# Performance work log

Hardware: AMD Instinct MI355X
Metric: run time of the kernel (lower is better)

The kernel has to match this reference:

```python
import jax, jax.numpy as jnp
import numpy as np

N_NODES = 10000
N_EDGES = 640000
NODE_DIM = 128
TIME_DIM = 64


def setup_inputs() -> dict:
    key = jax.random.key(0)
    ks = jax.random.split(key, 16)
    s = 0.05
    return {
        "h": jax.random.normal(ks[0], (N_NODES, NODE_DIM), jnp.float32),
        "diff_cart": jax.random.normal(ks[1], (N_EDGES, 3), jnp.float32),
        "dist_sq": jax.random.uniform(ks[2], (N_EDGES, 1), jnp.float32),
        "edge_src": jax.random.randint(ks[3], (N_EDGES,), 0, N_NODES),
        "edge_dst": jax.random.randint(ks[4], (N_EDGES,), 0, N_NODES),
        "t_emb_edges": jax.random.normal(ks[5], (N_EDGES, TIME_DIM), jnp.float32),
        "t_emb_nodes": jax.random.normal(ks[6], (N_NODES, TIME_DIM), jnp.float32),
        # edge_mlp: Linear(2*D+1+T -> D), SiLU, Linear(D -> D), SiLU
        "eW1": jax.random.normal(ks[7], (2 * NODE_DIM + 1 + TIME_DIM, NODE_DIM), jnp.float32) * s,
        "eb1": jnp.zeros((NODE_DIM,), jnp.float32),
        "eW2": jax.random.normal(ks[8], (NODE_DIM, NODE_DIM), jnp.float32) * s,
        "eb2": jnp.zeros((NODE_DIM,), jnp.float32),
        # coord_mlp: Linear(D -> D), SiLU, Linear(D -> 1, bias=False)
        "cW1": jax.random.normal(ks[9], (NODE_DIM, NODE_DIM), jnp.float32) * s,
        "cb1": jnp.zeros((NODE_DIM,), jnp.float32),
        "cW2": jax.random.normal(ks[10], (NODE_DIM, 1), jnp.float32) * s,
        # node_mlp: Linear(2*D+T -> D), SiLU, Linear(D -> D)
        "nW1": jax.random.normal(ks[11], (2 * NODE_DIM + TIME_DIM, NODE_DIM), jnp.float32) * s,
        "nb1": jnp.zeros((NODE_DIM,), jnp.float32),
        "nW2": jax.random.normal(ks[12], (NODE_DIM, NODE_DIM), jnp.float32) * s,
        "nb2": jnp.zeros((NODE_DIM,), jnp.float32),
    }


def reference(h, diff_cart, dist_sq, edge_src, edge_dst, t_emb_edges, t_emb_nodes,
              eW1, eb1, eW2, eb2, cW1, cb1, cW2, nW1, nb1, nW2, nb2):
    silu = jax.nn.silu
    n_nodes = h.shape[0]
    # gather + edge MLP: [E, 2D+1+T] -> [E, D]
    edge_in = jnp.concatenate([h[edge_src], h[edge_dst], dist_sq, t_emb_edges], axis=-1)
    m_ij = silu(silu(edge_in @ eW1 + eb1) @ eW2 + eb2)
    # coord MLP -> per-edge scalar weight [E, 1]
    coord_w = silu(m_ij @ cW1 + cb1) @ cW2
    # scatter-add coordinate shift onto source nodes [N, 3]
    coord_update = jax.ops.segment_sum(diff_cart * coord_w, edge_src, num_segments=n_nodes)
    # scatter-add messages onto destination nodes [N, D]
    m_i = jax.ops.segment_sum(m_ij, edge_dst, num_segments=n_nodes)
    # node MLP with residual
    node_in = jnp.concatenate([h, m_i, t_emb_nodes], axis=-1)
    h_update = h + (silu(node_in @ nW1 + nb1) @ nW2 + nb2)
    return h_update, coord_update
```

## Files before the change

kernel.cpp:

```cpp
#include <hip/hip_runtime.h>

typedef __bf16 bf16x8 __attribute__((ext_vector_type(8)));
typedef float f32x4 __attribute__((ext_vector_type(4)));
typedef unsigned short u16;

#define NN 10000
#define NE 640000
#define DIM 128
#define TD 64
#define LDT2 112
#define LDX 136
#define LDH 136

__device__ __forceinline__ u16 f2bf(float f){
    union { float f; unsigned u; } v; v.f = f;
    unsigned r = v.u + 0x7fffu + ((v.u >> 16) & 1u);
    return (u16)(r >> 16);
}
__device__ __forceinline__ unsigned f2bf2(float a, float b){
    unsigned r;
    asm("v_cvt_pk_bf16_f32 %0, %1, %2" : "=v"(r) : "v"(a), "v"(b));
    return r;
}
__device__ __forceinline__ float bfu2f(unsigned hs){
    union { unsigned u; float f; } v; v.u = hs << 16; return v.f;
}
__device__ __forceinline__ float silu_f(float x){ return x / (1.0f + __expf(-x)); }

__device__ __forceinline__ unsigned silu_add3_pk(unsigned xb, unsigned us, unsigned ud){
    float a0 = bfu2f(xb & 0xffffu) + bfu2f(us & 0xffffu) + bfu2f(ud & 0xffffu);
    float a1 = bfu2f(xb >> 16)     + bfu2f(us >> 16)     + bfu2f(ud >> 16);
    return f2bf2(silu_f(a0), silu_f(a1));
}

__global__ __launch_bounds__(256) void k_prep1(
    const float* __restrict__ eW1, const float* __restrict__ nW1,
    const float* __restrict__ eW2, const float* __restrict__ cW1,
    const float* __restrict__ nW2, const int* __restrict__ edst,
    u16* __restrict__ nW1t, u16* __restrict__ eW2t, u16* __restrict__ cW1t,
    u16* __restrict__ nW2t, u16* __restrict__ tWe2,
    u16* __restrict__ eW1tS, u16* __restrict__ eW1tD,
    int* __restrict__ deg, float* __restrict__ m_i, float* __restrict__ coord_out)
{
    int i = blockIdx.x * 256 + threadIdx.x;
    if (i < NE) {
        atomicAdd(&deg[edst[i]], 1);
        *reinterpret_cast<float2*>(m_i + (size_t)i * 2) = make_float2(0.f, 0.f);
    }
    if (i < NN * 3) coord_out[i] = 0.f;

    if (i < 40960) {
        int j = i / 320, k = i - j * 320;
        nW1t[i] = f2bf(nW1[k * DIM + j]);
    } else if (i < 57344) {
        int t = i - 40960; int j = t >> 7, k = t & 127;
        eW2t[t] = f2bf(eW2[k * DIM + j]);
    } else if (i < 73728) {
        int t = i - 57344; int j = t >> 7, k = t & 127;
        cW1t[t] = f2bf(cW1[k * DIM + j]);
    } else if (i < 90112) {
        int t = i - 73728; int j = t >> 7, k = t & 127;
        nW2t[t] = f2bf(nW2[k * DIM + j]);
    } else if (i < 102400) {
        int t = i - 90112; int j = t / 96, k = t - j * 96;
        float v = (k < 64) ? eW1[(257 + k) * DIM + j]
                 : (k == 64) ? eW1[256 * DIM + j] : 0.f;
        tWe2[t] = f2bf(v);
    } else if (i < 118784) {
        int t = i - 102400; int j = t >> 7, k = t & 127;
        eW1tS[t] = f2bf(eW1[k * DIM + j]);
    } else if (i < 135168) {
        int t = i - 118784; int j = t >> 7, k = t & 127;
        eW1tD[t] = f2bf(eW1[(128 + k) * DIM + j]);
    }
}

__global__ __launch_bounds__(256) void k_scan(const int* __restrict__ deg,
                                              int* __restrict__ offs, int* __restrict__ cursor){
    __shared__ int ps[256];
    int t = threadIdx.x;
    int base = t * 40, cnt = 0;
    if (t < 250) for (int i = 0; i < 40; ++i) cnt += deg[base + i];
    ps[t] = cnt; __syncthreads();
    for (int d = 1; d < 256; d <<= 1) {
        int v = (t >= d) ? ps[t - d] : 0;
        __syncthreads();
        ps[t] += v;
        __syncthreads();
    }
    int run = (t > 0) ? ps[t - 1] : 0;
    if (t < 250) for (int i = 0; i < 40; ++i) {
        offs[base + i] = run; cursor[base + i] = run; run += deg[base + i];
    }
    if (t == 0) offs[NN] = NE;
}

__global__ __launch_bounds__(256) void k_prep2(
    const float* __restrict__ h, const float* __restrict__ eb1,
    const u16* __restrict__ eW1tS, const u16* __restrict__ eW1tD,
    const int* __restrict__ esrc, const int* __restrict__ edst,
    const float* __restrict__ dist, const float* __restrict__ diffc,
    int* __restrict__ cursor,
    uint4* __restrict__ epack, float4* __restrict__ diff4,
    u16* __restrict__ H12)
{
    __shared__ u16 Hbuf[64 * LDH];
    const int tid = threadIdx.x;

    if (blockIdx.x < 2500) {
        int i = blockIdx.x * 256 + tid;
        if (i < NE) {
            int d = edst[i];
            int pos = atomicAdd(&cursor[d], 1);
            union { float f; unsigned u; } dv; dv.f = dist[i];
            epack[pos] = make_uint4((unsigned)esrc[i], (unsigned)d, dv.u, (unsigned)i);
            diff4[pos] = make_float4(diffc[(size_t)i * 3 + 0],
                                     diffc[(size_t)i * 3 + 1],
                                     diffc[(size_t)i * 3 + 2], 0.f);
        }
        return;
    }

    const int lane = tid & 63, w = tid >> 6;
    const int lo = lane & 15, hi = lane >> 4;
    const int nbase = (blockIdx.x - 2500) * 64;

    #pragma unroll
    for (int it = 0; it < 8; ++it) {
        int f = it * 256 + tid, e = f >> 5, c = f & 31;
        int node = nbase + e; if (node >= NN) node = NN - 1;
        float4 v = *reinterpret_cast<const float4*>(h + (size_t)node * DIM + c * 4);
        unsigned p0 = f2bf2(v.x, v.y), p1 = f2bf2(v.z, v.w);
        *reinterpret_cast<uint2*>(&Hbuf[e * LDH + c * 4]) = make_uint2(p0, p1);
    }
    __syncthreads();

    const u16* Wt = (w < 2) ? eW1tS : eW1tD;
    const int cc = (w & 1) * 64;
    f32x4 acc[4][4];
    #pragma unroll
    for (int rt = 0; rt < 4; ++rt)
        #pragma unroll
        for (int n = 0; n < 4; ++n) acc[rt][n] = f32x4{0.f,0.f,0.f,0.f};
    for (int ks = 0; ks < 4; ++ks) {
        bf16x8 a[4], b[4];
        #pragma unroll
        for (int rt = 0; rt < 4; ++rt)
            a[rt] = *reinterpret_cast<const bf16x8*>(&Hbuf[(rt*16+lo)*LDH + ks*32 + hi*8]);
        #pragma unroll
        for (int n = 0; n < 4; ++n)
            b[n] = *reinterpret_cast<const bf16x8*>(&Wt[(cc + n*16 + lo)*128 + ks*32 + hi*8]);
        #pragma unroll
        for (int rt = 0; rt < 4; ++rt)
            #pragma unroll
            for (int n = 0; n < 4; ++n)
                acc[rt][n] = __builtin_amdgcn_mfma_f32_16x16x32_bf16(a[rt], b[n], acc[rt][n], 0, 0, 0);
    }
    #pragma unroll
    for (int n = 0; n < 4; ++n) {
        int jloc = cc + n * 16 + lo;
        int j = ((w < 2) ? 0 : 128) + jloc;
        float bias = (w < 2) ? eb1[jloc] : 0.f;
        #pragma unroll
        for (int rt = 0; rt < 4; ++rt)
            #pragma unroll
            for (int r = 0; r < 4; ++r) {
                int node = nbase + rt * 16 + hi * 4 + r;
                if (node < NN) H12[(size_t)node * 256 + j] = f2bf(acc[rt][n][r] + bias);
            }
    }
}

__global__ __launch_bounds__(256, 8) void egnn_edge9(
    const uint4* __restrict__ epack, const float4* __restrict__ diff4,
    const float* __restrict__ tembE,
    const float* __restrict__ eb2, const float* __restrict__ cb1,
    const float* __restrict__ cW2,
    const u16* __restrict__ H12, const u16* __restrict__ tWe2,
    const u16* __restrict__ eW2t, const u16* __restrict__ cW1t,
    float* __restrict__ m_i, float* __restrict__ coord_out)
{
    __shared__ u16 B[64 * LDX];
    __shared__ int seid[64], srcv[64], dstv[64], flags[64];
    __shared__ float cwpart[4][64];

    const int tid = threadIdx.x, lane = tid & 63, w = tid >> 6;
    const int lo = lane & 15, hi = lane >> 4;
    const int bid = (blockIdx.x & 7) * 1250 + (blockIdx.x >> 3);
    const int ebase = bid * 64;
    const int colb = w * 32;
    const int col0 = colb + lo;

    float dl = 0.f;
    if (tid < 64) {
        uint4 ep = epack[ebase + tid];
        srcv[tid] = (int)ep.x;
        dstv[tid] = (int)ep.y;
        union { unsigned u; float f; } dv; dv.u = ep.z;
        dl = dv.f;
        seid[tid] = (int)ep.w;
    }
    __syncthreads();

    if (tid < 64) {
        flags[tid] = (tid == 63) || (dstv[tid] != dstv[tid + 1]);
        uint4 z0 = make_uint4((unsigned)f2bf(dl), 0u, 0u, 0u);
        uint4 zz = make_uint4(0u, 0u, 0u, 0u);
        *reinterpret_cast<uint4*>(&B[tid * LDT2 + 64]) = z0;
        *reinterpret_cast<uint4*>(&B[tid * LDT2 + 72]) = zz;
        *reinterpret_cast<uint4*>(&B[tid * LDT2 + 80]) = zz;
        *reinterpret_cast<uint4*>(&B[tid * LDT2 + 88]) = zz;
    }
    #pragma unroll
    for (int it = 0; it < 4; ++it) {
        int f = it * 256 + tid, e = f >> 4, c = f & 15;
        float4 v = *reinterpret_cast<const float4*>(tembE + (size_t)seid[e] * TD + c * 4);
        unsigned p0 = f2bf2(v.x, v.y), p1 = f2bf2(v.z, v.w);
        *reinterpret_cast<uint2*>(&B[e * LDT2 + c * 4]) = make_uint2(p0, p1);
    }
    __syncthreads();

    f32x4 acc[4][2];
    #pragma unroll
    for (int rt = 0; rt < 4; ++rt)
        #pragma unroll
        for (int n = 0; n < 2; ++n) acc[rt][n] = f32x4{0.f,0.f,0.f,0.f};
    #pragma unroll
    for (int ks = 0; ks < 3; ++ks) {
        bf16x8 a[4], b[2];
        #pragma unroll
        for (int rt = 0; rt < 4; ++rt)
            a[rt] = *reinterpret_cast<const bf16x8*>(&B[(rt*16+lo)*LDT2 + ks*32 + hi*8]);
        #pragma unroll
        for (int n = 0; n < 2; ++n)
            b[n] = *reinterpret_cast<const bf16x8*>(&tWe2[(colb + n*16 + lo)*96 + ks*32 + hi*8]);
        #pragma unroll
        for (int rt = 0; rt < 4; ++rt)
            #pragma unroll
            for (int n = 0; n < 2; ++n)
                acc[rt][n] = __builtin_amdgcn_mfma_f32_16x16x32_bf16(a[rt], b[n], acc[rt][n], 0, 0, 0);
    }
    __syncthreads();

    #pragma unroll
    for (int rt = 0; rt < 4; ++rt)
        #pragma unroll
        for (int n = 0; n < 2; ++n)
            #pragma unroll
            for (int r = 0; r < 4; ++r)
                B[(rt*16 + hi*4 + r) * LDX + colb + n*16 + lo] = f2bf(acc[rt][n][r]);
    __syncthreads();

    {
        int row = tid >> 2, q = tid & 3;
        int sv = srcv[row], dv = dstv[row];
        const uint4* hs = reinterpret_cast<const uint4*>(H12 + (size_t)sv * 256 + q * 32);
        const uint4* hd = reinterpret_cast<const uint4*>(H12 + (size_t)dv * 256 + 128 + q * 32);
        uint4* bp = reinterpret_cast<uint4*>(&B[row * LDX + q * 32]);
        #pragma unroll
        for (int c4 = 0; c4 < 4; ++c4) {
            uint4 xb = bp[c4];
            uint4 us = hs[c4];
            uint4 ud = hd[c4];
            uint4 o;
            o.x = silu_add3_pk(xb.x, us.x, ud.x);
            o.y = silu_add3_pk(xb.y, us.y, ud.y);
            o.z = silu_add3_pk(xb.z, us.z, ud.z);
            o.w = silu_add3_pk(xb.w, us.w, ud.w);
            bp[c4] = o;
        }
    }
    __syncthreads();

    #pragma unroll
    for (int rt = 0; rt < 4; ++rt)
        #pragma unroll
        for (int n = 0; n < 2; ++n) acc[rt][n] = f32x4{0.f,0.f,0.f,0.f};
    #pragma unroll
    for (int ks = 0; ks < 4; ++ks) {
        bf16x8 a[4], b[2];
        #pragma unroll
        for (int rt = 0; rt < 4; ++rt)
            a[rt] = *reinterpret_cast<const bf16x8*>(&B[(rt*16+lo)*LDX + ks*32 + hi*8]);
        #pragma unroll
        for (int n = 0; n < 2; ++n)
            b[n] = *reinterpret_cast<const bf16x8*>(&eW2t[(colb + n*16 + lo)*128 + ks*32 + hi*8]);
        #pragma unroll
        for (int rt = 0; rt < 4; ++rt)
            #pragma unroll
            for (int n = 0; n < 2; ++n)
                acc[rt][n] = __builtin_amdgcn_mfma_f32_16x16x32_bf16(a[rt], b[n], acc[rt][n], 0, 0, 0);
    }
    __syncthreads();

    {
        float b20 = eb2[col0], b21 = eb2[col0 + 16];
        #pragma unroll
        for (int rt = 0; rt < 4; ++rt)
            #pragma unroll
            for (int r = 0; r < 4; ++r) {
                int row = rt * 16 + hi * 4 + r;
                unsigned p = f2bf2(silu_f(acc[rt][0][r] + b20), silu_f(acc[rt][1][r] + b21));
                B[row * LDX + col0]      = (u16)p;
                B[row * LDX + col0 + 16] = (u16)(p >> 16);
            }
    }
    __syncthreads();

    #pragma unroll
    for (int rt = 0; rt < 4; ++rt)
        #pragma unroll
        for (int n = 0; n < 2; ++n) acc[rt][n] = f32x4{0.f,0.f,0.f,0.f};
    #pragma unroll
    for (int ks = 0; ks < 4; ++ks) {
        bf16x8 a[4], b[2];
        #pragma unroll
        for (int rt = 0; rt < 4; ++rt)
            a[rt] = *reinterpret_cast<const bf16x8*>(&B[(rt*16+lo)*LDX + ks*32 + hi*8]);
        #pragma unroll
        for (int n = 0; n < 2; ++n)
            b[n] = *reinterpret_cast<const bf16x8*>(&cW1t[(colb + n*16 + lo)*128 + ks*32 + hi*8]);
        #pragma unroll
        for (int rt = 0; rt < 4; ++rt)
            #pragma unroll
            for (int n = 0; n < 2; ++n)
                acc[rt][n] = __builtin_amdgcn_mfma_f32_16x16x32_bf16(a[rt], b[n], acc[rt][n], 0, 0, 0);
    }
    {
        float b30 = cb1[col0], b31 = cb1[col0 + 16];
        float c20 = cW2[col0], c21 = cW2[col0 + 16];
        #pragma unroll
        for (int rt = 0; rt < 4; ++rt)
            #pragma unroll
            for (int r = 0; r < 4; ++r) {
                float p = silu_f(acc[rt][0][r] + b30) * c20
                        + silu_f(acc[rt][1][r] + b31) * c21;
                p += __shfl_xor(p, 1, 16);
                p += __shfl_xor(p, 2, 16);
                p += __shfl_xor(p, 4, 16);
                p += __shfl_xor(p, 8, 16);
                if (lo == 0) cwpart[w][rt * 16 + hi * 4 + r] = p;
            }
    }

    {
        int cp = (tid & 63) * 2, rh = tid >> 6;
        float s0 = 0.f, s1 = 0.f;
        #pragma unroll
        for (int r = 0; r < 16; ++r) {
            int row = rh * 16 + r;
            unsigned u = *reinterpret_cast<const unsigned*>(&B[row * LDX + cp]);
            s0 += bfu2f(u & 0xffffu); s1 += bfu2f(u >> 16);
            if (flags[row]) {
                unsafeAtomicAdd(&m_i[(size_t)dstv[row] * DIM + cp],     s0);
                unsafeAtomicAdd(&m_i[(size_t)dstv[row] * DIM + cp + 1], s1);
                s0 = 0.f; s1 = 0.f;
            }
        }
        if (s0 != 0.f || s1 != 0.f) {
            int lr = rh * 16 + 15;
            unsafeAtomicAdd(&m_i[(size_t)dstv[lr] * DIM + cp],     s0);
            unsafeAtomicAdd(&m_i[(size_t)dstv[lr] * DIM + cp + 1], s1);
        }
    }
    __syncthreads();

    if (tid < 192) {
        int e = tid / 3, c = tid - e * 3;
        float cw = cwpart[0][e] + cwpart[1][e] + cwpart[2][e] + cwpart[3][e];
        float val = reinterpret_cast<const float*>(diff4 + (size_t)(ebase + e))[c] * cw;
        unsafeAtomicAdd(coord_out + (size_t)srcv[e] * 3 + c, val);
    }
}

__global__ __launch_bounds__(256) void egnn_node(
    const float* __restrict__ h, const float* __restrict__ m_i,
    const float* __restrict__ tembN,
    const float* __restrict__ nb1, const float* __restrict__ nb2,
    const u16* __restrict__ nW1t, const u16* __restrict__ nW2t,
    float* __restrict__ out)
{
    __shared__ u16 Abuf[64 * 328];
    __shared__ u16 Xbuf[64 * LDX];

    const int tid = threadIdx.x, lane = tid & 63, w = tid >> 6;
    const int lo = lane & 15, hi = lane >> 4;
    const int nbase = blockIdx.x * 64;

    #pragma unroll
    for (int it = 0; it < 8; ++it) {
        int f = it * 256 + tid, e = f >> 5, c = f & 31;
        int node = nbase + e; if (node >= NN) node = NN - 1;
        float4 v = *reinterpret_cast<const float4*>(h + (size_t)node * DIM + c * 4);
        unsigned p0 = f2bf2(v.x, v.y), p1 = f2bf2(v.z, v.w);
        *reinterpret_cast<uint2*>(&Abuf[e * 328 + c * 4]) = make_uint2(p0, p1);
        float4 v2 = *reinterpret_cast<const float4*>(m_i + (size_t)node * DIM + c * 4);
        unsigned q0 = f2bf2(v2.x, v2.y), q1 = f2bf2(v2.z, v2.w);
        *reinterpret_cast<uint2*>(&Abuf[e * 328 + 128 + c * 4]) = make_uint2(q0, q1);
    }
    #pragma unroll
    for (int it = 0; it < 4; ++it) {
        int f = it * 256 + tid, e = f >> 4, c = f & 15;
        int node = nbase + e; if (node >= NN) node = NN - 1;
        float4 v = *reinterpret_cast<const float4*>(tembN + (size_t)node * TD + c * 4);
        unsigned p0 = f2bf2(v.x, v.y), p1 = f2bf2(v.z, v.w);
        *reinterpret_cast<uint2*>(&Abuf[e * 328 + 256 + c * 4]) = make_uint2(p0, p1);
    }
    __syncthreads();

    const int colb = w * 32;
    f32x4 acc[4][2];

    #pragma unroll
    for (int rt = 0; rt < 4; ++rt)
        #pragma unroll
        for (int n = 0; n < 2; ++n) acc[rt][n] = f32x4{0.f,0.f,0.f,0.f};
    for (int ks = 0; ks < 10; ++ks) {
        bf16x8 a[4], b[2];
        #pragma unroll
        for (int rt = 0; rt < 4; ++rt)
            a[rt] = *reinterpret_cast<const bf16x8*>(&Abuf[(rt*16+lo)*328 + ks*32 + hi*8]);
        #pragma unroll
        for (int n = 0; n < 2; ++n)
            b[n] = *reinterpret_cast<const bf16x8*>(&nW1t[(colb + n*16 + lo)*320 + ks*32 + hi*8]);
        #pragma unroll
        for (int rt = 0; rt < 4; ++rt)
            #pragma unroll
            for (int n = 0; n < 2; ++n)
                acc[rt][n] = __builtin_amdgcn_mfma_f32_16x16x32_bf16(a[rt], b[n], acc[rt][n], 0, 0, 0);
    }
    {
        float bias1[2];
        #pragma unroll
        for (int n = 0; n < 2; ++n) bias1[n] = nb1[colb + n*16 + lo];
        #pragma unroll
        for (int rt = 0; rt < 4; ++rt)
            #pragma unroll
            for (int n = 0; n < 2; ++n)
                #pragma unroll
                for (int r = 0; r < 4; ++r) {
                    int row = rt * 16 + hi * 4 + r;
                    Xbuf[row * LDX + colb + n*16 + lo] = f2bf(silu_f(acc[rt][n][r] + bias1[n]));
                }
    }
    __syncthreads();

    #pragma unroll
    for (int rt = 0; rt < 4; ++rt)
        #pragma unroll
        for (int n = 0; n < 2; ++n) acc[rt][n] = f32x4{0.f,0.f,0.f,0.f};
    #pragma unroll
    for (int ks = 0; ks < 4; ++ks) {
        bf16x8 a[4], b[2];
        #pragma unroll
        for (int rt = 0; rt < 4; ++rt)
            a[rt] = *reinterpret_cast<const bf16x8*>(&Xbuf[(rt*16+lo)*LDX + ks*32 + hi*8]);
        #pragma unroll
        for (int n = 0; n < 2; ++n)
            b[n] = *reinterpret_cast<const bf16x8*>(&nW2t[(colb + n*16 + lo)*128 + ks*32 + hi*8]);
        #pragma unroll
        for (int rt = 0; rt < 4; ++rt)
            #pragma unroll
            for (int n = 0; n < 2; ++n)
                acc[rt][n] = __builtin_amdgcn_mfma_f32_16x16x32_bf16(a[rt], b[n], acc[rt][n], 0, 0, 0);
    }
    {
        float bias2[2];
        #pragma unroll
        for (int n = 0; n < 2; ++n) bias2[n] = nb2[colb + n*16 + lo];
        #pragma unroll
        for (int rt = 0; rt < 4; ++rt)
            #pragma unroll
            for (int n = 0; n < 2; ++n)
                #pragma unroll
                for (int r = 0; r < 4; ++r) {
                    int row = rt * 16 + hi * 4 + r;
                    int node = nbase + row;
                    if (node < NN) {
                        int col = colb + n * 16 + lo;
                        out[(size_t)node * DIM + col] =
                            acc[rt][n][r] + bias2[n] + h[(size_t)node * DIM + col];
                    }
                }
    }
}

extern "C" void kernel_launch(void* const* d_in, const int* in_sizes, int n_in,
                              void* d_out, int out_size, void* d_ws, size_t ws_size,
                              hipStream_t stream)
{
    const float* h     = (const float*)d_in[0];
    const float* diffc = (const float*)d_in[1];
    const float* dist  = (const float*)d_in[2];
    const int*   esrc  = (const int*)d_in[3];
    const int*   edst  = (const int*)d_in[4];
    const float* tembE = (const float*)d_in[5];
    const float* tembN = (const float*)d_in[6];
    const float* eW1   = (const float*)d_in[7];
    const float* eb1   = (const float*)d_in[8];
    const float* eW2   = (const float*)d_in[9];
    const float* eb2   = (const float*)d_in[10];
    const float* cW1   = (const float*)d_in[11];
    const float* cb1   = (const float*)d_in[12];
    const float* cW2   = (const float*)d_in[13];
    const float* nW1   = (const float*)d_in[14];
    const float* nb1   = (const float*)d_in[15];
    const float* nW2   = (const float*)d_in[16];
    const float* nb2   = (const float*)d_in[17];

    char* ws = (char*)d_ws;
    u16*   H12    = (u16*)(ws + 0);
    float* m_i    = (float*)(ws + 5120000);
    u16*   tWe2   = (u16*)(ws + 10240000);
    u16*   eW1tS  = (u16*)(ws + 10264576);
    u16*   eW1tD  = (u16*)(ws + 10297344);
    u16*   eW2t   = (u16*)(ws + 10330112);
    u16*   cW1t   = (u16*)(ws + 10362880);
    u16*   nW1t   = (u16*)(ws + 10395648);
    u16*   nW2t   = (u16*)(ws + 10477568);
    int*   deg    = (int*)(ws + 10510336);
    int*   offs   = (int*)(ws + 10550400);
    int*   cursor = (int*)(ws + 10590464);
    uint4* epack  = (uint4*)(ws + 10630528);
    float4* diff4 = (float4*)(ws + 20870528);

    float* outp      = (float*)d_out;
    float* coord_out = outp + (size_t)NN * DIM;

    hipMemsetAsync(deg, 0, 40064, stream);

    k_prep1<<<2500, 256, 0, stream>>>(eW1, nW1, eW2, cW1, nW2, edst,
                                      nW1t, eW2t, cW1t, nW2t, tWe2, eW1tS, eW1tD,
                                      deg, m_i, coord_out);
    k_scan<<<1, 256, 0, stream>>>(deg, offs, cursor);
    k_prep2<<<2500 + (NN + 63) / 64, 256, 0, stream>>>(h, eb1, eW1tS, eW1tD,
                                                       esrc, edst, dist, diffc,
                                                       cursor, epack, diff4, H12);
    egnn_edge9<<<NE / 64, 256, 0, stream>>>(epack, diff4, tembE, eb2, cb1, cW2,
                                            H12, tWe2, eW2t, cW1t, m_i, coord_out);
    egnn_node<<<(NN + 63) / 64, 256, 0, stream>>>(h, m_i, tembN, nb1, nb2,
                                                  nW1t, nW2t, outp);
}
```

Baseline: 305.1 us.

## Fuse layer-1 epilogue into registers using permuted H12 and eW2 layouts

Stores the precomputed per-node H12 projections as packed bf16 pairs in an MFMA-output-friendly column order. The edge kernel then adds the src/dst contributions directly to accumulator registers, applies SiLU, and writes LDS once. This removes an LDS write, a barrier and an LDS read-modify-write pass. eW2 rows are permuted to match the interleaved column order, and launch bounds drop from 8 to 6 waves per SIMD, which raises the register budget but lowers occupancy. Gathers become 4-byte per-lane loads per row instead of 16-byte vector loads, so memory coalescing may get worse.

```diff
diff --git a/kernel.cpp b/kernel.cpp
--- a/kernel.cpp
+++ b/kernel.cpp
@@ -27,17 +27,15 @@
 }
 __device__ __forceinline__ float silu_f(float x){ return x / (1.0f + __expf(-x)); }
 
-__device__ __forceinline__ unsigned silu_add3_pk(unsigned xb, unsigned us, unsigned ud){
-    float a0 = bfu2f(xb & 0xffffu) + bfu2f(us & 0xffffu) + bfu2f(ud & 0xffffu);
-    float a1 = bfu2f(xb >> 16)     + bfu2f(us >> 16)     + bfu2f(ud >> 16);
-    return f2bf2(silu_f(a0), silu_f(a1));
+__device__ __forceinline__ int korig(int kp){
+    return (kp & ~31) + ((kp & 1) << 4) + ((kp & 31) >> 1);
 }
 
 __global__ __launch_bounds__(256) void k_prep1(
     const float* __restrict__ eW1, const float* __restrict__ nW1,
     const float* __restrict__ eW2, const float* __restrict__ cW1,
     const float* __restrict__ nW2, const int* __restrict__ edst,
-    u16* __restrict__ nW1t, u16* __restrict__ eW2t, u16* __restrict__ cW1t,
+    u16* __restrict__ nW1t, u16* __restrict__ eW2tP, u16* __restrict__ cW1t,
     u16* __restrict__ nW2t, u16* __restrict__ tWe2,
     u16* __restrict__ eW1tS, u16* __restrict__ eW1tD,
     int* __restrict__ deg, float* __restrict__ m_i, float* __restrict__ coord_out)
@@ -53,8 +51,8 @@
         int j = i / 320, k = i - j * 320;
         nW1t[i] = f2bf(nW1[k * DIM + j]);
     } else if (i < 57344) {
-        int t = i - 40960; int j = t >> 7, k = t & 127;
-        eW2t[t] = f2bf(eW2[k * DIM + j]);
+        int t = i - 40960; int j = t >> 7, kp = t & 127;
+        eW2tP[t] = f2bf(eW2[korig(kp) * DIM + j]);
     } else if (i < 73728) {
         int t = i - 57344; int j = t >> 7, k = t & 127;
         cW1t[t] = f2bf(cW1[k * DIM + j]);
@@ -102,7 +100,7 @@
     const float* __restrict__ dist, const float* __restrict__ diffc,
     int* __restrict__ cursor,
     uint4* __restrict__ epack, float4* __restrict__ diff4,
-    u16* __restrict__ H12)
+    unsigned* __restrict__ H12p)
 {
     __shared__ u16 Hbuf[64 * LDH];
     const int tid = threadIdx.x;
@@ -156,28 +154,32 @@
             for (int n = 0; n < 4; ++n)
                 acc[rt][n] = __builtin_amdgcn_mfma_f32_16x16x32_bf16(a[rt], b[n], acc[rt][n], 0, 0, 0);
     }
-    #pragma unroll
-    for (int n = 0; n < 4; ++n) {
-        int jloc = cc + n * 16 + lo;
-        int j = ((w < 2) ? 0 : 128) + jloc;
-        float bias = (w < 2) ? eb1[jloc] : 0.f;
+    const int base = (w < 2) ? 0 : 64;
+    #pragma unroll
+    for (int n = 0; n < 4; n += 2) {
+        int c0 = cc + n * 16 + lo;
+        int u32i = (cc >> 1) + ((n >> 1) << 4) + lo;
+        float b0 = (w < 2) ? eb1[c0] : 0.f;
+        float b1 = (w < 2) ? eb1[c0 + 16] : 0.f;
         #pragma unroll
         for (int rt = 0; rt < 4; ++rt)
             #pragma unroll
             for (int r = 0; r < 4; ++r) {
                 int node = nbase + rt * 16 + hi * 4 + r;
-                if (node < NN) H12[(size_t)node * 256 + j] = f2bf(acc[rt][n][r] + bias);
+                if (node < NN)
+                    H12p[(size_t)node * 128 + base + u32i] =
+                        f2bf2(acc[rt][n][r] + b0, acc[rt][n + 1][r] + b1);
             }
     }
 }
 
-__global__ __launch_bounds__(256, 8) void egnn_edge9(
+__global__ __launch_bounds__(256, 6) void egnn_edge10(
     const uint4* __restrict__ epack, const float4* __restrict__ diff4,
     const float* __restrict__ tembE,
     const float* __restrict__ eb2, const float* __restrict__ cb1,
     const float* __restrict__ cW2,
-    const u16* __restrict__ H12, const u16* __restrict__ tWe2,
-    const u16* __restrict__ eW2t, const u16* __restrict__ cW1t,
+    const unsigned* __restrict__ H12p, const u16* __restrict__ tWe2,
+    const u16* __restrict__ eW2tP, const u16* __restrict__ cW1t,
     float* __restrict__ m_i, float* __restrict__ coord_out)
 {
     __shared__ u16 B[64 * LDX];
@@ -242,33 +244,20 @@
     }
     __syncthreads();
 
-    #pragma unroll
-    for (int rt = 0; rt < 4; ++rt)
-        #pragma unroll
-        for (int n = 0; n < 2; ++n)
-            #pragma unroll
-            for (int r = 0; r < 4; ++r)
-                B[(rt*16 + hi*4 + r) * LDX + colb + n*16 + lo] = f2bf(acc[rt][n][r]);
-    __syncthreads();
-
     {
-        int row = tid >> 2, q = tid & 3;
-        int sv = srcv[row], dv = dstv[row];
-        const uint4* hs = reinterpret_cast<const uint4*>(H12 + (size_t)sv * 256 + q * 32);
-        const uint4* hd = reinterpret_cast<const uint4*>(H12 + (size_t)dv * 256 + 128 + q * 32);
-        uint4* bp = reinterpret_cast<uint4*>(&B[row * LDX + q * 32]);
-        #pragma unroll
-        for (int c4 = 0; c4 < 4; ++c4) {
-            uint4 xb = bp[c4];
-            uint4 us = hs[c4];
-            uint4 ud = hd[c4];
-            uint4 o;
-            o.x = silu_add3_pk(xb.x, us.x, ud.x);
-            o.y = silu_add3_pk(xb.y, us.y, ud.y);
-            o.z = silu_add3_pk(xb.z, us.z, ud.z);
-            o.w = silu_add3_pk(xb.w, us.w, ud.w);
-            bp[c4] = o;
-        }
+        const int u32i = (colb >> 1) + lo;
+        #pragma unroll
+        for (int rt = 0; rt < 4; ++rt)
+            #pragma unroll
+            for (int r = 0; r < 4; ++r) {
+                int row = rt * 16 + hi * 4 + r;
+                unsigned us = H12p[(size_t)srcv[row] * 128 + u32i];
+                unsigned ud = H12p[(size_t)dstv[row] * 128 + 64 + u32i];
+                float x0 = acc[rt][0][r] + bfu2f(us & 0xffffu) + bfu2f(ud & 0xffffu);
+                float x1 = acc[rt][1][r] + bfu2f(us >> 16)     + bfu2f(ud >> 16);
+                *reinterpret_cast<unsigned*>(&B[row * LDX + colb + lo * 2])
+                    = f2bf2(silu_f(x0), silu_f(x1));
+            }
     }
     __syncthreads();
 
@@ -284,7 +273,7 @@
             a[rt] = *reinterpret_cast<const bf16x8*>(&B[(rt*16+lo)*LDX + ks*32 + hi*8]);
         #pragma unroll
         for (int n = 0; n < 2; ++n)
-            b[n] = *reinterpret_cast<const bf16x8*>(&eW2t[(colb + n*16 + lo)*128 + ks*32 + hi*8]);
+            b[n] = *reinterpret_cast<const bf16x8*>(&eW2tP[(colb + n*16 + lo)*128 + ks*32 + hi*8]);
         #pragma unroll
         for (int rt = 0; rt < 4; ++rt)
             #pragma unroll
@@ -509,12 +498,12 @@
     const float* nb2   = (const float*)d_in[17];
 
     char* ws = (char*)d_ws;
-    u16*   H12    = (u16*)(ws + 0);
+    unsigned* H12p = (unsigned*)(ws + 0);
     float* m_i    = (float*)(ws + 5120000);
     u16*   tWe2   = (u16*)(ws + 10240000);
     u16*   eW1tS  = (u16*)(ws + 10264576);
     u16*   eW1tD  = (u16*)(ws + 10297344);
-    u16*   eW2t   = (u16*)(ws + 10330112);
+    u16*   eW2tP  = (u16*)(ws + 10330112);
     u16*   cW1t   = (u16*)(ws + 10362880);
     u16*   nW1t   = (u16*)(ws + 10395648);
     u16*   nW2t   = (u16*)(ws + 10477568);
@@ -530,14 +519,14 @@
     hipMemsetAsync(deg, 0, 40064, stream);
 
     k_prep1<<<2500, 256, 0, stream>>>(eW1, nW1, eW2, cW1, nW2, edst,
-                                      nW1t, eW2t, cW1t, nW2t, tWe2, eW1tS, eW1tD,
+                                      nW1t, eW2tP, cW1t, nW2t, tWe2, eW1tS, eW1tD,
                                       deg, m_i, coord_out);
     k_scan<<<1, 256, 0, stream>>>(deg, offs, cursor);
     k_prep2<<<2500 + (NN + 63) / 64, 256, 0, stream>>>(h, eb1, eW1tS, eW1tD,
                                                        esrc, edst, dist, diffc,
-                                                       cursor, epack, diff4, H12);
-    egnn_edge9<<<NE / 64, 256, 0, stream>>>(epack, diff4, tembE, eb2, cb1, cW2,
-                                            H12, tWe2, eW2t, cW1t, m_i, coord_out);
+                                                       cursor, epack, diff4, H12p);
+    egnn_edge10<<<NE / 64, 256, 0, stream>>>(epack, diff4, tembE, eb2, cb1, cW2,
+                                             H12p, tWe2, eW2tP, cW1t, m_i, coord_out);
     egnn_node<<<(NN + 63) / 64, 256, 0, stream>>>(h, m_i, tembN, nb1, nb2,
                                                   nW1t, nW2t, outp);
 }
```

Result: no change. 310.0 us (+1.6%).
